# Performance work log

Measured on AMD Instinct MI355X. Metric: run time of the kernel, lower is better.

Reference implementation:

```python
import jax, jax.numpy as jnp
import numpy as np

N = 50000   # num_nodes
T = 24      # window_size
H = 64      # hidden_dim
HOR = 12    # horizon
E = 1600000 # num edges


def setup_inputs() -> dict:
    key = jax.random.key(0)
    ks = jax.random.split(key, 12)
    s = 1.0 / np.sqrt(H)
    u = lambda k, shape: jax.random.uniform(k, shape, jnp.float32, -s, s)
    return {
        "x": jax.random.normal(ks[0], (N, T), jnp.float32),
        "edge_index": jax.random.randint(ks[1], (2, E), 0, N, dtype=jnp.int32),
        "w_ih": u(ks[2], (3 * H, 1)),
        "w_hh": u(ks[3], (3 * H, H)),
        "b_ih": u(ks[4], (3 * H,)),
        "b_hh": u(ks[5], (3 * H,)),
        "gc1_w": u(ks[6], (H, H)),
        "gc1_b": u(ks[7], (H,)),
        "gc2_w": u(ks[8], (H, H)),
        "gc2_b": u(ks[9], (H,)),
        "fc_w": u(ks[10], (HOR, H)),
        "fc_b": u(ks[11], (HOR,)),
    }


def _gru_last(x, w_ih, w_hh, b_ih, b_hh):
    # x: [N, T] scalar-per-step input (input_size=1). Returns final hidden [N, H].
    h0 = jnp.zeros((x.shape[0], H), x.dtype)

    def step(h, xt):  # xt: [N]
        gi = xt[:, None] * w_ih[:, 0][None, :] + b_ih   # [N, 3H]
        gh = h @ w_hh.T + b_hh                          # [N, 3H]
        i_r, i_z, i_n = jnp.split(gi, 3, axis=-1)
        h_r, h_z, h_n = jnp.split(gh, 3, axis=-1)
        r = jax.nn.sigmoid(i_r + h_r)
        z = jax.nn.sigmoid(i_z + h_z)
        n = jnp.tanh(i_n + r * h_n)
        h = (1.0 - z) * n + z * h
        return h, None

    hT, _ = jax.lax.scan(step, h0, x.T)  # scan over time axis
    return hT


def _gcn_norm(edge_index, n):
    # PyG GCNConv: add self loops, symmetric D^-1/2 (A+I) D^-1/2 normalization.
    loops = jnp.arange(n, dtype=edge_index.dtype)
    src = jnp.concatenate([edge_index[0], loops])
    dst = jnp.concatenate([edge_index[1], loops])
    deg = jax.ops.segment_sum(jnp.ones(src.shape, jnp.float32), dst, num_segments=n)
    dinv = jnp.where(deg > 0, jax.lax.rsqrt(jnp.maximum(deg, 1e-12)), 0.0)
    return src, dst, dinv[src] * dinv[dst]


def _gcn(h, src, dst, norm, W, b, n):
    hw = h @ W.T                      # [N, H] linear transform first
    msg = hw[src] * norm[:, None]     # gather + edge weighting
    return jax.ops.segment_sum(msg, dst, num_segments=n) + b


def reference(x, edge_index, w_ih, w_hh, b_ih, b_hh, gc1_w, gc1_b, gc2_w, gc2_b, fc_w, fc_b):
    n = x.shape[0]
    h = _gru_last(x, w_ih, w_hh, b_ih, b_hh)            # [N, H] last GRU output
    src, dst, norm = _gcn_norm(edge_index, n)
    h = jax.nn.relu(_gcn(h, src, dst, norm, gc1_w, gc1_b, n))
    h = jax.nn.relu(_gcn(h, src, dst, norm, gc2_w, gc2_b, n))
    return h @ fc_w.T + fc_b                            # [N, HOR]
```

## Files before the change

kernel.cpp:

```cpp
#include <hip/hip_runtime.h>

#define NN 50000
#define TT 24
#define HH 64
#define HORZ 12
#define EE 1600000

#define GP 256
#define EP (EE / GP)
#define BK 784
#define NBG (BK * GP)
#define SCB (NBG / 512)
#define BKA ((NN + 63) / 64)

typedef __attribute__((ext_vector_type(8))) _Float16 f16x8;
typedef __attribute__((ext_vector_type(4))) float f32x4;

__device__ __forceinline__ float sigm(float x) {
  return __builtin_amdgcn_rcpf(1.f + __expf(-x));
}
__device__ __forceinline__ float tanh_f(float x) {
  return 1.f - 2.f * __builtin_amdgcn_rcpf(1.f + __expf(2.f * x));
}

__global__ void build_frags_kernel(const float* __restrict__ whh, const float* __restrict__ g1,
                                   const float* __restrict__ g2, const float* __restrict__ fcw,
                                   _Float16* __restrict__ frag) {
  int idx = blockIdx.x * 256 + threadIdx.x;
  if (idx >= 21504) return;
  const float* W;
  int rows, li;
  if (idx < 12288) { W = whh; rows = 192; li = idx; }
  else if (idx < 16384) { W = g1; rows = 64; li = idx - 12288; }
  else if (idx < 20480) { W = g2; rows = 64; li = idx - 16384; }
  else { W = fcw; rows = HORZ; li = idx - 20480; }
  int j = li & 7;
  int l = (li >> 3) & 63;
  int kf = (li >> 9) & 1;
  int nf = li >> 10;
  int col = 16 * nf + (l & 15);
  int k = 32 * kf + 8 * (l >> 4) + j;
  frag[idx] = (col < rows) ? (_Float16)W[col * 64 + k] : (_Float16)0.f;
}

__global__ __launch_bounds__(256) void p1_hist_kernel(const int* __restrict__ dst,
                                                      int* __restrict__ hist) {
  __shared__ int h[BK];
  int tid = threadIdx.x, g = blockIdx.x;
  for (int b = tid; b < BK; b += 256) h[b] = 0;
  __syncthreads();
  int e0 = g * EP;
  for (int i = tid; i < EP; i += 256) atomicAdd(&h[dst[e0 + i] >> 6], 1);
  __syncthreads();
  for (int b = tid; b < BK; b += 256) hist[b * GP + g] = h[b];
}

__global__ void scanA_kernel(const int* __restrict__ v, int* __restrict__ part) {
  __shared__ int s[512];
  int i = blockIdx.x * 512 + threadIdx.x;
  s[threadIdx.x] = v[i];
  __syncthreads();
  for (int off = 256; off > 0; off >>= 1) {
    if (threadIdx.x < off) s[threadIdx.x] += s[threadIdx.x + off];
    __syncthreads();
  }
  if (threadIdx.x == 0) part[blockIdx.x] = s[0];
}

__global__ void scanB_kernel(int* __restrict__ part) {
  __shared__ int s[512];
  int t = threadIdx.x;
  int v = (t < SCB) ? part[t] : 0;
  s[t] = v;
  __syncthreads();
  for (int off = 1; off < 512; off <<= 1) {
    int a = s[t];
    int b = (t >= off) ? s[t - off] : 0;
    __syncthreads();
    s[t] = a + b;
    __syncthreads();
  }
  if (t < SCB) part[t] = s[t] - v;
}

__global__ void scanC_kernel(int* __restrict__ cellbase, const int* __restrict__ part) {
  __shared__ int s[2][512];
  int tid = threadIdx.x;
  int i = blockIdx.x * 512 + tid;
  int x = cellbase[i];
  s[0][tid] = x;
  __syncthreads();
  int cur = 0;
  for (int off = 1; off < 512; off <<= 1) {
    int nxt = cur ^ 1;
    int val = s[cur][tid] + ((tid >= off) ? s[cur][tid - off] : 0);
    s[nxt][tid] = val;
    __syncthreads();
    cur = nxt;
  }
  cellbase[i] = part[blockIdx.x] + s[cur][tid] - x;
  if (i == 0) cellbase[NBG] = EE;
}

__global__ __launch_bounds__(256) void p2_scatter_kernel(
    const int* __restrict__ src, const int* __restrict__ dst,
    const int* __restrict__ cellbase, unsigned int* __restrict__ rec) {
  __shared__ int cur[BK];
  int tid = threadIdx.x, g = blockIdx.x;
  for (int b = tid; b < BK; b += 256) cur[b] = cellbase[b * GP + g];
  __syncthreads();
  int e0 = g * EP;
  for (int i = tid; i < EP; i += 256) {
    int e = e0 + i;
    int d = dst[e];
    int s = src[e];
    int p = atomicAdd(&cur[d >> 6], 1);
    rec[p] = ((unsigned)(d & 63) << 16) | (unsigned)s;
  }
}

__global__ __launch_bounds__(256) void sort2_kernel(
    const unsigned int* __restrict__ rec, const int* __restrict__ cellbase,
    unsigned short* __restrict__ csr, int* __restrict__ row_start,
    float* __restrict__ dinv) {
  __shared__ int cnt[64];
  __shared__ int cur[64];
  int b = blockIdx.x, tid = threadIdx.x;
  if (tid < 64) cnt[tid] = 0;
  __syncthreads();
  int e0 = cellbase[b * GP], e1 = cellbase[(b + 1) * GP];
  for (int e = e0 + tid; e < e1; e += 256) atomicAdd(&cnt[rec[e] >> 16], 1);
  __syncthreads();
  if (tid == 0) {
    int a = e0;
#pragma unroll
    for (int l = 0; l < 64; ++l) { int c = cnt[l]; cur[l] = a; a += c; }
  }
  __syncthreads();
  if (tid < 64) {
    int n = b * 64 + tid;
    if (n <= NN) row_start[n] = cur[tid];
    if (n < NN) dinv[n] = rsqrtf((float)(cnt[tid] + 1));
  }
  __syncthreads();
  for (int e = e0 + tid; e < e1; e += 256) {
    unsigned int r = rec[e];
    int p = atomicAdd(&cur[r >> 16], 1);
    csr[p] = (unsigned short)(r & 0xFFFFu);
  }
}

__global__ __launch_bounds__(256, 4) void gru_kernel(
    const float* __restrict__ x, const float* __restrict__ w_ih,
    const float* __restrict__ b_ih, const float* __restrict__ b_hh,
    const _Float16* __restrict__ wfrag, const _Float16* __restrict__ l1f,
    const float* __restrict__ dinv, _Float16* __restrict__ hw) {
  __shared__ __align__(16) _Float16 sh[2][2][16][72];
  __shared__ __align__(16) float xs[2][TT][16];

  const int tid = threadIdx.x;
  const int lane = tid & 63;
  const int w = tid >> 6;
  const int c = lane & 15;
  const int q = lane >> 4;
  const int d = 16 * w + c;

  f16x8 Br0 = *(const f16x8*)&wfrag[(((w)*2 + 0) * 64 + lane) * 8];
  f16x8 Br1 = *(const f16x8*)&wfrag[(((w)*2 + 1) * 64 + lane) * 8];
  f16x8 Bz0 = *(const f16x8*)&wfrag[(((4 + w) * 2 + 0) * 64 + lane) * 8];
  f16x8 Bz1 = *(const f16x8*)&wfrag[(((4 + w) * 2 + 1) * 64 + lane) * 8];
  f16x8 Bn0 = *(const f16x8*)&wfrag[(((8 + w) * 2 + 0) * 64 + lane) * 8];
  f16x8 Bn1 = *(const f16x8*)&wfrag[(((8 + w) * 2 + 1) * 64 + lane) * 8];

  const float wir = w_ih[d], wiz = w_ih[64 + d], win = w_ih[128 + d];
  const float arb = b_ih[d] + b_hh[d];
  const float azb = b_ih[64 + d] + b_hh[64 + d];
  const float bin = b_ih[128 + d];
  const float bhn = b_hh[128 + d];

  const int base = blockIdx.x * 32;

  for (int i = tid; i < 32 * TT; i += 256) {
    int nl = i / TT;
    int t = i - nl * TT;
    int node = base + nl;
    xs[nl >> 4][t][nl & 15] = (node < NN) ? x[node * TT + t] : 0.f;
  }
  __syncthreads();

  float hreg[2][4];
#pragma unroll
  for (int g = 0; g < 2; ++g)
#pragma unroll
    for (int r = 0; r < 4; ++r) hreg[g][r] = 0.f;

#pragma unroll 1
  for (int t = 0; t < TT; ++t) {
#pragma unroll
    for (int g = 0; g < 2; ++g) {
      f32x4 ar = (f32x4){arb, arb, arb, arb};
      f32x4 az = (f32x4){azb, azb, azb, azb};
      f32x4 an = (f32x4){bhn, bhn, bhn, bhn};
      if (t > 0) {
        const _Float16* S = &sh[(t & 1) ^ 1][g][0][0];
        f16x8 a0 = *(const f16x8*)&S[c * 72 + 8 * q];
        f16x8 a1 = *(const f16x8*)&S[c * 72 + 32 + 8 * q];
        ar = __builtin_amdgcn_mfma_f32_16x16x32_f16(a0, Br0, ar, 0, 0, 0);
        az = __builtin_amdgcn_mfma_f32_16x16x32_f16(a0, Bz0, az, 0, 0, 0);
        an = __builtin_amdgcn_mfma_f32_16x16x32_f16(a0, Bn0, an, 0, 0, 0);
        ar = __builtin_amdgcn_mfma_f32_16x16x32_f16(a1, Br1, ar, 0, 0, 0);
        az = __builtin_amdgcn_mfma_f32_16x16x32_f16(a1, Bz1, az, 0, 0, 0);
        an = __builtin_amdgcn_mfma_f32_16x16x32_f16(a1, Bn1, an, 0, 0, 0);
      }
      float4 xt = *(const float4*)&xs[g][t][4 * q];
      float xv[4] = {xt.x, xt.y, xt.z, xt.w};
#pragma unroll
      for (int r = 0; r < 4; ++r) {
        float rg = sigm(xv[r] * wir + ar[r]);
        float zg = sigm(xv[r] * wiz + az[r]);
        float nn = tanh_f(rg * an[r] + (xv[r] * win + bin));
        float hn = nn + zg * (hreg[g][r] - nn);
        hreg[g][r] = hn;
        sh[t & 1][g][4 * q + r][d] = (_Float16)hn;
      }
    }
    __syncthreads();
  }

  f16x8 L0 = *(const f16x8*)&l1f[((w * 2 + 0) * 64 + lane) * 8];
  f16x8 L1 = *(const f16x8*)&l1f[((w * 2 + 1) * 64 + lane) * 8];
#pragma unroll
  for (int g = 0; g < 2; ++g) {
    const _Float16* S = &sh[1][g][0][0];
    f16x8 a0 = *(const f16x8*)&S[c * 72 + 8 * q];
    f16x8 a1 = *(const f16x8*)&S[c * 72 + 32 + 8 * q];
    f32x4 acc = (f32x4){0.f, 0.f, 0.f, 0.f};
    acc = __builtin_amdgcn_mfma_f32_16x16x32_f16(a0, L0, acc, 0, 0, 0);
    acc = __builtin_amdgcn_mfma_f32_16x16x32_f16(a1, L1, acc, 0, 0, 0);
#pragma unroll
    for (int r = 0; r < 4; ++r) {
      int n = base + 16 * g + 4 * q + r;
      if (n < NN) hw[n * 64 + d] = (_Float16)(acc[r] * dinv[n]);
    }
  }
}

__global__ __launch_bounds__(1024, 4) void agg_lin_kernel(
    const _Float16* __restrict__ hwp, const float* __restrict__ dinv,
    const int* __restrict__ row_start, const unsigned short* __restrict__ csr,
    const float* __restrict__ bias, const _Float16* __restrict__ l2f,
    _Float16* __restrict__ out) {
  __shared__ __align__(16) _Float16 h1[64][72];
  int tid = threadIdx.x, b = blockIdx.x;
  int wv = tid >> 6, lane = tid & 63;
  float bl = bias[lane];
#pragma unroll 1
  for (int k = 0; k < 4; ++k) {
    int row = wv * 4 + k;
    int n = b * 64 + row;
    float v = 0.f;
    if (n < NN) {
      int e0 = row_start[n], e1 = row_start[n + 1];
      float a0 = (float)hwp[n * 64 + lane];
      float a1 = 0.f, a2 = 0.f, a3 = 0.f;
      int e = e0;
      for (; e < e1 && (e & 7); ++e) a0 += (float)hwp[(int)csr[e] * 64 + lane];
      for (; e + 8 <= e1; e += 8) {
        uint4 pk = *(const uint4*)&csr[e];
        a0 += (float)hwp[(pk.x & 0xFFFF) * 64 + lane];
        a1 += (float)hwp[(pk.x >> 16) * 64 + lane];
        a2 += (float)hwp[(pk.y & 0xFFFF) * 64 + lane];
        a3 += (float)hwp[(pk.y >> 16) * 64 + lane];
        a0 += (float)hwp[(pk.z & 0xFFFF) * 64 + lane];
        a1 += (float)hwp[(pk.z >> 16) * 64 + lane];
        a2 += (float)hwp[(pk.w & 0xFFFF) * 64 + lane];
        a3 += (float)hwp[(pk.w >> 16) * 64 + lane];
      }
      for (; e < e1; ++e) a0 += (float)hwp[(int)csr[e] * 64 + lane];
      v = (a0 + a1 + a2 + a3) * dinv[n] + bl;
      v = v > 0.f ? v : 0.f;
    }
    h1[row][lane] = (_Float16)v;
  }
  __syncthreads();
  int g = wv >> 2, wq = wv & 3;
  int c = lane & 15, q = lane >> 4;
  f16x8 B0 = *(const f16x8*)&l2f[((wq * 2 + 0) * 64 + lane) * 8];
  f16x8 B1 = *(const f16x8*)&l2f[((wq * 2 + 1) * 64 + lane) * 8];
  f16x8 a0 = *(const f16x8*)&h1[16 * g + c][8 * q];
  f16x8 a1 = *(const f16x8*)&h1[16 * g + c][32 + 8 * q];
  f32x4 acc = (f32x4){0.f, 0.f, 0.f, 0.f};
  acc = __builtin_amdgcn_mfma_f32_16x16x32_f16(a0, B0, acc, 0, 0, 0);
  acc = __builtin_amdgcn_mfma_f32_16x16x32_f16(a1, B1, acc, 0, 0, 0);
#pragma unroll
  for (int r = 0; r < 4; ++r) {
    int n = b * 64 + 16 * g + 4 * q + r;
    if (n < NN) out[n * 64 + 16 * wq + c] = (_Float16)(acc[r] * dinv[n]);
  }
}

__global__ __launch_bounds__(1024, 4) void agg_fc_kernel(
    const _Float16* __restrict__ hwp, const float* __restrict__ dinv,
    const int* __restrict__ row_start, const unsigned short* __restrict__ csr,
    const float* __restrict__ bias, const _Float16* __restrict__ fcf,
    const float* __restrict__ fcb, float* __restrict__ out) {
  __shared__ __align__(16) _Float16 h1[64][72];
  int tid = threadIdx.x, b = blockIdx.x;
  int wv = tid >> 6, lane = tid & 63;
  float bl = bias[lane];
#pragma unroll 1
  for (int k = 0; k < 4; ++k) {
    int row = wv * 4 + k;
    int n = b * 64 + row;
    float v = 0.f;
    if (n < NN) {
      int e0 = row_start[n], e1 = row_start[n + 1];
      float a0 = (float)hwp[n * 64 + lane];
      float a1 = 0.f, a2 = 0.f, a3 = 0.f;
      int e = e0;
      for (; e < e1 && (e & 7); ++e) a0 += (float)hwp[(int)csr[e] * 64 + lane];
      for (; e + 8 <= e1; e += 8) {
        uint4 pk = *(const uint4*)&csr[e];
        a0 += (float)hwp[(pk.x & 0xFFFF) * 64 + lane];
        a1 += (float)hwp[(pk.x >> 16) * 64 + lane];
        a2 += (float)hwp[(pk.y & 0xFFFF) * 64 + lane];
        a3 += (float)hwp[(pk.y >> 16) * 64 + lane];
        a0 += (float)hwp[(pk.z & 0xFFFF) * 64 + lane];
        a1 += (float)hwp[(pk.z >> 16) * 64 + lane];
        a2 += (float)hwp[(pk.w & 0xFFFF) * 64 + lane];
        a3 += (float)hwp[(pk.w >> 16) * 64 + lane];
      }
      for (; e < e1; ++e) a0 += (float)hwp[(int)csr[e] * 64 + lane];
      v = (a0 + a1 + a2 + a3) * dinv[n] + bl;
      v = v > 0.f ? v : 0.f;
    }
    h1[row][lane] = (_Float16)v;
  }
  __syncthreads();
  if (wv < 4) {
    int g = wv;
    int c = lane & 15, q = lane >> 4;
    f16x8 B0 = *(const f16x8*)&fcf[(0 * 64 + lane) * 8];
    f16x8 B1 = *(const f16x8*)&fcf[(1 * 64 + lane) * 8];
    f16x8 a0 = *(const f16x8*)&h1[16 * g + c][8 * q];
    f16x8 a1 = *(const f16x8*)&h1[16 * g + c][32 + 8 * q];
    float bc = (c < HORZ) ? fcb[c] : 0.f;
    f32x4 acc = (f32x4){bc, bc, bc, bc};
    acc = __builtin_amdgcn_mfma_f32_16x16x32_f16(a0, B0, acc, 0, 0, 0);
    acc = __builtin_amdgcn_mfma_f32_16x16x32_f16(a1, B1, acc, 0, 0, 0);
    if (c < HORZ) {
#pragma unroll
      for (int r = 0; r < 4; ++r) {
        int n = b * 64 + 16 * g + 4 * q + r;
        if (n < NN) out[n * HORZ + c] = acc[r];
      }
    }
  }
}

extern "C" void kernel_launch(void* const* d_in, const int* in_sizes, int n_in,
                              void* d_out, int out_size, void* d_ws, size_t ws_size,
                              hipStream_t stream) {
  (void)in_sizes; (void)n_in; (void)out_size; (void)ws_size;
  const float* x = (const float*)d_in[0];
  const int* edge_index = (const int*)d_in[1];
  const float* w_ih = (const float*)d_in[2];
  const float* w_hh = (const float*)d_in[3];
  const float* b_ih = (const float*)d_in[4];
  const float* b_hh = (const float*)d_in[5];
  const float* gc1_w = (const float*)d_in[6];
  const float* gc1_b = (const float*)d_in[7];
  const float* gc2_w = (const float*)d_in[8];
  const float* gc2_b = (const float*)d_in[9];
  const float* fc_w = (const float*)d_in[10];
  const float* fc_b = (const float*)d_in[11];
  float* out = (float*)d_out;

  char* ws = (char*)d_ws;
  _Float16* wfrag = (_Float16*)ws;
  _Float16* l1f = wfrag + 12288;
  _Float16* l2f = l1f + 4096;
  _Float16* fcf = l2f + 4096;
  _Float16* hw1 = (_Float16*)(ws + 43008);
  _Float16* hw2 = hw1 + NN * 64;
  float* dinv = (float*)(hw2 + NN * 64);
  int* row_start = (int*)(dinv + NN);
  int* cellbase = row_start + 50240;
  int* part = cellbase + NBG + 4;
  unsigned int* rec = (unsigned int*)(part + 512);
  unsigned short* csr = (unsigned short*)(rec + EE);

  const int* esrc = edge_index;
  const int* edst = edge_index + EE;

  build_frags_kernel<<<84, 256, 0, stream>>>(w_hh, gc1_w, gc2_w, fc_w, wfrag);
  p1_hist_kernel<<<GP, 256, 0, stream>>>(edst, cellbase);
  scanA_kernel<<<SCB, 512, 0, stream>>>(cellbase, part);
  scanB_kernel<<<1, 512, 0, stream>>>(part);
  scanC_kernel<<<SCB, 512, 0, stream>>>(cellbase, part);
  p2_scatter_kernel<<<GP, 256, 0, stream>>>(esrc, edst, cellbase, rec);
  sort2_kernel<<<BK, 256, 0, stream>>>(rec, cellbase, csr, row_start, dinv);

  gru_kernel<<<(NN + 31) / 32, 256, 0, stream>>>(x, w_ih, b_ih, b_hh, wfrag, l1f, dinv, hw1);
  agg_lin_kernel<<<BKA, 1024, 0, stream>>>(hw1, dinv, row_start, csr, gc1_b, l2f, hw2);
  agg_fc_kernel<<<BKA, 1024, 0, stream>>>(hw2, dinv, row_start, csr, gc2_b, fcf, fc_b, out);
}
```

Measured before the change: 263.9 us.

## Shrink GRU blocks to 16 nodes and raise occupancy target

Each GRU block now processes one 16-node group instead of two, so twice as many blocks launch and the launch bound allows 8 blocks per CU. Shared memory per block halves and the node bounds checks are dropped because the node count divides evenly by 16. The goal is more resident waves to hide the latency of the sequential recurrence. In exchange, the two independent groups that previously interleaved inside a block are lost, and there are now twice as many block-wide barriers overall.

After: 276.3 us. +4.7%, slower.

```diff
diff --git a/kernel.cpp b/kernel.cpp
--- a/kernel.cpp
+++ b/kernel.cpp
@@ -150,13 +150,13 @@
   }
 }
 
-__global__ __launch_bounds__(256, 4) void gru_kernel(
+__global__ __launch_bounds__(256, 8) void gru_kernel(
     const float* __restrict__ x, const float* __restrict__ w_ih,
     const float* __restrict__ b_ih, const float* __restrict__ b_hh,
     const _Float16* __restrict__ wfrag, const _Float16* __restrict__ l1f,
     const float* __restrict__ dinv, _Float16* __restrict__ hw) {
-  __shared__ __align__(16) _Float16 sh[2][2][16][72];
-  __shared__ __align__(16) float xs[2][TT][16];
+  __shared__ __align__(16) _Float16 sh[2][16][72];
+  __shared__ __align__(16) float xs[TT][16];
 
   const int tid = threadIdx.x;
   const int lane = tid & 63;
@@ -178,31 +178,27 @@
   const float bin = b_ih[128 + d];
   const float bhn = b_hh[128 + d];
 
-  const int base = blockIdx.x * 32;
-
-  for (int i = tid; i < 32 * TT; i += 256) {
+  const int base = blockIdx.x * 16;
+
+  for (int i = tid; i < 16 * TT; i += 256) {
     int nl = i / TT;
     int t = i - nl * TT;
-    int node = base + nl;
-    xs[nl >> 4][t][nl & 15] = (node < NN) ? x[node * TT + t] : 0.f;
-  }
-  __syncthreads();
-
-  float hreg[2][4];
-#pragma unroll
-  for (int g = 0; g < 2; ++g)
-#pragma unroll
-    for (int r = 0; r < 4; ++r) hreg[g][r] = 0.f;
+    xs[t][nl] = x[(base + nl) * TT + t];
+  }
+  __syncthreads();
+
+  float hreg[4] = {0.f, 0.f, 0.f, 0.f};
 
 #pragma unroll 1
-  for (int t = 0; t < TT; ++t) {
-#pragma unroll
-    for (int g = 0; g < 2; ++g) {
+  for (int tp = 0; tp < TT / 2; ++tp) {
+#pragma unroll
+    for (int half = 0; half < 2; ++half) {
+      const int t = 2 * tp + half;
       f32x4 ar = (f32x4){arb, arb, arb, arb};
       f32x4 az = (f32x4){azb, azb, azb, azb};
       f32x4 an = (f32x4){bhn, bhn, bhn, bhn};
       if (t > 0) {
-        const _Float16* S = &sh[(t & 1) ^ 1][g][0][0];
+        const _Float16* S = &sh[half ^ 1][0][0];
         f16x8 a0 = *(const f16x8*)&S[c * 72 + 8 * q];
         f16x8 a1 = *(const f16x8*)&S[c * 72 + 32 + 8 * q];
         ar = __builtin_amdgcn_mfma_f32_16x16x32_f16(a0, Br0, ar, 0, 0, 0);
@@ -212,26 +208,25 @@
         az = __builtin_amdgcn_mfma_f32_16x16x32_f16(a1, Bz1, az, 0, 0, 0);
         an = __builtin_amdgcn_mfma_f32_16x16x32_f16(a1, Bn1, an, 0, 0, 0);
       }
-      float4 xt = *(const float4*)&xs[g][t][4 * q];
+      float4 xt = *(const float4*)&xs[t][4 * q];
       float xv[4] = {xt.x, xt.y, xt.z, xt.w};
 #pragma unroll
       for (int r = 0; r < 4; ++r) {
         float rg = sigm(xv[r] * wir + ar[r]);
         float zg = sigm(xv[r] * wiz + az[r]);
         float nn = tanh_f(rg * an[r] + (xv[r] * win + bin));
-        float hn = nn + zg * (hreg[g][r] - nn);
-        hreg[g][r] = hn;
-        sh[t & 1][g][4 * q + r][d] = (_Float16)hn;
+        float hn = nn + zg * (hreg[r] - nn);
+        hreg[r] = hn;
+        sh[half][4 * q + r][d] = (_Float16)hn;
       }
+      __syncthreads();
     }
-    __syncthreads();
   }
 
   f16x8 L0 = *(const f16x8*)&l1f[((w * 2 + 0) * 64 + lane) * 8];
   f16x8 L1 = *(const f16x8*)&l1f[((w * 2 + 1) * 64 + lane) * 8];
-#pragma unroll
-  for (int g = 0; g < 2; ++g) {
-    const _Float16* S = &sh[1][g][0][0];
+  {
+    const _Float16* S = &sh[1][0][0];
     f16x8 a0 = *(const f16x8*)&S[c * 72 + 8 * q];
     f16x8 a1 = *(const f16x8*)&S[c * 72 + 32 + 8 * q];
     f32x4 acc = (f32x4){0.f, 0.f, 0.f, 0.f};
@@ -239,8 +234,8 @@
     acc = __builtin_amdgcn_mfma_f32_16x16x32_f16(a1, L1, acc, 0, 0, 0);
 #pragma unroll
     for (int r = 0; r < 4; ++r) {
-      int n = base + 16 * g + 4 * q + r;
-      if (n < NN) hw[n * 64 + d] = (_Float16)(acc[r] * dinv[n]);
+      int n = base + 4 * q + r;
+      hw[n * 64 + d] = (_Float16)(acc[r] * dinv[n]);
     }
   }
 }
@@ -401,7 +396,7 @@
   p2_scatter_kernel<<<GP, 256, 0, stream>>>(esrc, edst, cellbase, rec);
   sort2_kernel<<<BK, 256, 0, stream>>>(rec, cellbase, csr, row_start, dinv);
 
-  gru_kernel<<<(NN + 31) / 32, 256, 0, stream>>>(x, w_ih, b_ih, b_hh, wfrag, l1f, dinv, hw1);
+  gru_kernel<<<NN / 16, 256, 0, stream>>>(x, w_ih, b_ih, b_hh, wfrag, l1f, dinv, hw1);
   agg_lin_kernel<<<BKA, 1024, 0, stream>>>(hw1, dinv, row_start, csr, gc1_b, l2f, hw2);
   agg_fc_kernel<<<BKA, 1024, 0, stream>>>(hw2, dinv, row_start, csr, gc2_b, fcf, fc_b, out);
 }
```
